# Kernel optimization log

Measured on AMD Instinct MI355X. Metric: run time of the kernel, lower is better.

Reference implementation:

```python
import jax, jax.numpy as jnp
import numpy as np

N, E, B = 50000, 400000, 8
ND, ED, H, L = 32, 16, 128, 3

def setup_inputs() -> dict:
    key = jax.random.key(0)
    ks = jax.random.split(key, 32)
    s = 0.05
    inp = {
        'x': jax.random.normal(ks[0], (N, ND), jnp.float32),
        'edge_attr': jax.random.normal(ks[1], (E, ED), jnp.float32),
        'global_feature': jax.random.normal(ks[2], (B, 1), jnp.float32),
        'edge_index': jax.random.randint(ks[3], (2, E), 0, N, jnp.int64),
        'batch': jnp.sort(jax.random.randint(ks[4], (N,), 0, B, jnp.int64)),
        # embeddings
        'Wn': jax.random.normal(ks[5], (ND, H), jnp.float32) * s,
        'bn': jnp.zeros((H,), jnp.float32),
        'We': jax.random.normal(ks[6], (ED, H), jnp.float32) * s,
        'be': jnp.zeros((H,), jnp.float32),
        'Wg': jax.random.normal(ks[7], (1, H), jnp.float32) * s,
        'bg': jnp.zeros((H,), jnp.float32),
        # message-passing layers (stacked over L)
        'mW1': jax.random.normal(ks[8], (L, 3 * H, H), jnp.float32) * s,
        'mb1': jnp.zeros((L, H), jnp.float32),
        'mW2': jax.random.normal(ks[9], (L, H, H), jnp.float32) * s,
        'mb2': jnp.zeros((L, H), jnp.float32),
        'uW1': jax.random.normal(ks[10], (L, 2 * H, H), jnp.float32) * s,
        'ub1': jnp.zeros((L, H), jnp.float32),
        'uW2': jax.random.normal(ks[11], (L, H, H), jnp.float32) * s,
        'ub2': jnp.zeros((L, H), jnp.float32),
        # readout MLP
        'rW1': jax.random.normal(ks[12], (2 * H, H), jnp.float32) * s,
        'rb1': jnp.zeros((H,), jnp.float32),
        'rW2': jax.random.normal(ks[13], (H, H // 2), jnp.float32) * s,
        'rb2': jnp.zeros((H // 2,), jnp.float32),
        'rW3': jax.random.normal(ks[14], (H // 2, 1), jnp.float32) * s,
        'rb3': jnp.zeros((1,), jnp.float32),
    }
    return inp

def reference(x, edge_attr, global_feature, Wn, bn, We, be, Wg, bg,
              mW1, mb1, mW2, mb2, uW1, ub1, uW2, ub2,
              rW1, rb1, rW2, rb2, rW3, rb3, edge_index, batch):
    h = x @ Wn + bn                      # [N,H]
    e = edge_attr @ We + be              # [E,H]
    g = global_feature @ Wg + bg         # [B,H]
    src, dst = edge_index[0], edge_index[1]  # PyG: x_j=source, x_i=target, aggregate at target
    for l in range(L):
        m_in = jnp.concatenate([h[dst], h[src], e], axis=1)            # [E,3H]
        m = jax.nn.relu(m_in @ mW1[l] + mb1[l]) @ mW2[l] + mb2[l]       # [E,H]
        aggr = jax.ops.segment_sum(m, dst, num_segments=N)              # [N,H]
        u_in = jnp.concatenate([h, aggr], axis=1)                       # [N,2H]
        upd = jax.nn.relu(u_in @ uW1[l] + ub1[l]) @ uW2[l] + ub2[l]
        h = h + upd
    counts = jax.ops.segment_sum(jnp.ones((N,), h.dtype), batch, num_segments=B)
    pooled = jax.ops.segment_sum(h, batch, num_segments=B) / jnp.maximum(counts, 1.0)[:, None]
    final = jnp.concatenate([pooled, g], axis=1)                        # [B,2H]
    out = jax.nn.relu(final @ rW1 + rb1)
    out = jax.nn.relu(out @ rW2 + rb2)
    return out @ rW3 + rb3                                              # [B,1]
```

## Files before the change

### kernel.cpp

```cpp
#include <hip/hip_runtime.h>

#define NN 50000
#define NPAD 50048
#define NBLK 391
#define NE 400000
#define NBATCH 8
#define NDIM 32
#define EDIM 16
#define H 128
#define NLAYERS 3
#define CHUNK_ELEMS 4096
#define NODE_CHUNKS 24
#define ZW_CHUNK 8192
#define NSB 196
#define ZEB 128

typedef __attribute__((ext_vector_type(8))) __bf16 bf16x8;
typedef __attribute__((ext_vector_type(16))) float f32x16;
typedef __attribute__((ext_vector_type(8))) short short8;
typedef __attribute__((ext_vector_type(2))) float v2f;

__device__ __forceinline__ void block_sync_lds() {
  asm volatile("s_waitcnt lgkmcnt(0)\ns_barrier" ::: "memory");
}
__device__ __forceinline__ void wait_lds() {
  asm volatile("s_waitcnt lgkmcnt(0)" ::: "memory");
}
__device__ __forceinline__ v2f bf2f(unsigned u) {
  v2f r;
  r.x = __uint_as_float(u << 16);
  r.y = __uint_as_float(u & 0xffff0000u);
  return r;
}

__global__ __launch_bounds__(128) void embed_nodes_kernel(
    const float* __restrict__ x, const float* __restrict__ Wn,
    const float* __restrict__ bn, __bf16* __restrict__ hb) {
  __shared__ float Ws[NDIM * H];
  __shared__ float xs[16 * NDIM];
  int j = threadIdx.x;
  int nbase = blockIdx.x * 16;
  for (int r = 0; r < NDIM; ++r) Ws[r * H + j] = Wn[r * H + j];
#pragma unroll
  for (int t = 0; t < 4; ++t) {
    int f = j + t * 128;
    xs[f] = x[nbase * NDIM + f];
  }
  __syncthreads();
  float b = bn[j];
  for (int nn = 0; nn < 16; ++nn) {
    float acc = b;
#pragma unroll
    for (int k = 0; k < NDIM; ++k)
      acc = fmaf(xs[nn * NDIM + k], Ws[k * H + j], acc);
    hb[(size_t)(nbase + nn) * H + j] = (__bf16)acc;
  }
}

__global__ __launch_bounds__(256) void degree_kernel(const int* __restrict__ ei,
                                                     int* __restrict__ deg) {
  int e = blockIdx.x * 256 + threadIdx.x;
  if (e < NE) atomicAdd(&deg[ei[NE + e]], 1);
}

__global__ __launch_bounds__(256) void scan1_kernel(const int* __restrict__ deg,
                                                    int* __restrict__ bsum) {
  __shared__ int ws[4];
  int i = blockIdx.x * 256 + threadIdx.x;
  int lane = threadIdx.x & 63, wid = threadIdx.x >> 6;
  int v = (i < NN) ? deg[i] : 0;
#pragma unroll
  for (int off = 32; off; off >>= 1) v += __shfl_down(v, off);
  if (lane == 0) ws[wid] = v;
  __syncthreads();
  if (threadIdx.x == 0) bsum[blockIdx.x] = ws[0] + ws[1] + ws[2] + ws[3];
}

__global__ __launch_bounds__(256) void scan2_kernel(const int* __restrict__ bsum,
                                                    int* __restrict__ boff) {
  __shared__ int s[256];
  int t = threadIdx.x;
  int v = (t < NSB) ? bsum[t] : 0;
  s[t] = v;
  __syncthreads();
  for (int off = 1; off < 256; off <<= 1) {
    int u = (t >= off) ? s[t - off] : 0;
    __syncthreads();
    s[t] += u;
    __syncthreads();
  }
  if (t < NSB) boff[t] = s[t] - v;
}

__global__ __launch_bounds__(256) void scan3_kernel(const int* __restrict__ deg,
                                                    const int* __restrict__ boff,
                                                    int* __restrict__ cursor) {
  __shared__ int wsum[4], woff[4];
  int i = blockIdx.x * 256 + threadIdx.x;
  int lane = threadIdx.x & 63, wid = threadIdx.x >> 6;
  int orig = (i < NN) ? deg[i] : 0;
  int v = orig;
#pragma unroll
  for (int off = 1; off < 64; off <<= 1) {
    int u = __shfl_up(v, off);
    if (lane >= off) v += u;
  }
  if (lane == 63) wsum[wid] = v;
  __syncthreads();
  if (threadIdx.x == 0) {
    int r = 0;
#pragma unroll
    for (int w = 0; w < 4; ++w) {
      woff[w] = r;
      r += wsum[w];
    }
  }
  __syncthreads();
  if (i < NN) cursor[i] = (v - orig) + woff[wid] + boff[blockIdx.x];
}

__global__ __launch_bounds__(256) void scatter_kernel(
    const int* __restrict__ ei, int* __restrict__ cursor,
    int* __restrict__ srcSrt, int* __restrict__ eidSrt) {
  int e = blockIdx.x * 256 + threadIdx.x;
  if (e < NE) {
    int d = ei[NE + e];
    int pos = atomicAdd(&cursor[d], 1);
    srcSrt[pos] = ei[e];
    eidSrt[pos] = e;
  }
}

__global__ __launch_bounds__(256) void gather_ea_kernel(
    const float* __restrict__ ea, const int* __restrict__ eidSrt,
    __bf16* __restrict__ eaSrt) {
  int fl = blockIdx.x * 256 + threadIdx.x;
  if (fl < NE) {
    int e = eidSrt[fl];
    const float4* ep = (const float4*)(ea + (size_t)e * EDIM);
    __bf16* op = eaSrt + (size_t)fl * EDIM;
#pragma unroll
    for (int q = 0; q < 4; ++q) {
      float4 v = ep[q];
      op[q * 4 + 0] = (__bf16)v.x;
      op[q * 4 + 1] = (__bf16)v.y;
      op[q * 4 + 2] = (__bf16)v.z;
      op[q * 4 + 3] = (__bf16)v.w;
    }
  }
}

__global__ __launch_bounds__(256) void precomp_zw_kernel(
    const float* __restrict__ mW1, __bf16* __restrict__ ZW) {
  int l = blockIdx.x / 8;
  int c = blockIdx.x % 8;
  int tid = threadIdx.x;
  const float* w1 = mW1 + (size_t)l * 384 * H;
  __bf16* dst = ZW + ((size_t)l * 8 + c) * ZW_CHUNK;
  for (int it = 0; it < 32; ++it) {
    int flat = it * 256 + tid;
    int j = flat & 7;
    int lane = (flat >> 3) & 63;
    int nt = (flat >> 9) & 7;
    int hilo = flat >> 12;
    int k = c * 16 + ((lane >> 5) << 3) + j;
    int n = nt * 32 + (lane & 31);
    float w = (n < 128) ? w1[(size_t)k * H + n]
                        : w1[(size_t)(128 + k) * H + (n - 128)];
    __bf16 hi = (__bf16)w;
    __bf16 lo = (__bf16)(w - (float)hi);
    dst[flat] = hilo ? lo : hi;
  }
}

__global__ __launch_bounds__(128) void precomp_wef_kernel(
    const float* __restrict__ mW1, const float* __restrict__ mb1,
    const float* __restrict__ We, const float* __restrict__ be,
    float* __restrict__ Wef, float* __restrict__ bm) {
  int l = blockIdx.x;
  int n = threadIdx.x;
  const float* w1 = mW1 + (size_t)l * 384 * H;
  float acc[EDIM];
#pragma unroll
  for (int i = 0; i < EDIM; ++i) acc[i] = 0.f;
  float accb = 0.f;
  for (int c = 0; c < H; ++c) {
    float wv = w1[(size_t)(256 + c) * H + n];
    accb = fmaf(be[c], wv, accb);
#pragma unroll
    for (int i = 0; i < EDIM; ++i)
      acc[i] = fmaf(We[i * H + c], wv, acc[i]);
  }
#pragma unroll
  for (int i = 0; i < EDIM; ++i)
    Wef[((size_t)l * EDIM + i) * H + n] = acc[i];
  bm[l * H + n] = mb1[l * H + n] + accb;
}

__global__ __launch_bounds__(256) void precomp_wefs_kernel(
    const float* __restrict__ Wef, __bf16* __restrict__ WefS) {
  int l = blockIdx.x;
  int tid = threadIdx.x;
  int nt = tid >> 6, lane = tid & 63;
  int n = nt * 32 + (lane & 31);
  int half = lane >> 5;
  const float* wl = Wef + (size_t)l * EDIM * H;
  __bf16* dst = WefS + (size_t)l * CHUNK_ELEMS;
#pragma unroll
  for (int j = 0; j < 8; ++j) {
    int k = half * 8 + j;
    float w = wl[(size_t)k * H + n];
    __bf16 hi = (__bf16)w;
    __bf16 lo = (__bf16)(w - (float)hi);
    dst[((0 * 4 + nt) * 64 + lane) * 8 + j] = hi;
    dst[((1 * 4 + nt) * 64 + lane) * 8 + j] = lo;
  }
}

__global__ __launch_bounds__(128) void precomp_wu_kernel(
    const float* __restrict__ uW1, const float* __restrict__ mW2,
    const float* __restrict__ mb2, float* __restrict__ Wu,
    float* __restrict__ va) {
  int l = blockIdx.x / 257;
  int r = blockIdx.x % 257;
  int j = threadIdx.x;
  const float* u1 = uW1 + (size_t)l * 256 * H;
  if (r < 128) {
    Wu[((size_t)l * 256 + r) * H + j] = u1[(size_t)r * H + j];
  } else if (r < 256) {
    int i = r - 128;
    const float* m2 = mW2 + ((size_t)l * H + i) * H;
    float s = 0.f;
    for (int c = 0; c < H; ++c)
      s = fmaf(m2[c], u1[(size_t)(128 + c) * H + j], s);
    Wu[((size_t)l * 256 + r) * H + j] = s;
  } else {
    float s = 0.f;
    for (int c = 0; c < H; ++c)
      s = fmaf(mb2[l * H + c], u1[(size_t)(128 + c) * H + j], s);
    va[l * H + j] = s;
  }
}

__global__ __launch_bounds__(256) void precomp_wns_kernel(
    const float* __restrict__ Wu, const float* __restrict__ uW2,
    __bf16* __restrict__ WnS) {
  int l = blockIdx.x / NODE_CHUNKS;
  int c = blockIdx.x % NODE_CHUNKS;
  int tid = threadIdx.x;
  int nt = tid >> 6, lane = tid & 63;
  int n = nt * 32 + (lane & 31);
  int half = lane >> 5;
  __bf16* dst = WnS + ((size_t)l * NODE_CHUNKS + c) * CHUNK_ELEMS;
#pragma unroll
  for (int j = 0; j < 8; ++j) {
    float w;
    if (c < 16) {
      int k = c * 16 + half * 8 + j;
      w = Wu[((size_t)l * 256 + k) * H + n];
    } else {
      int k = (c - 16) * 16 + half * 8 + j;
      w = uW2[((size_t)l * H + k) * H + n];
    }
    __bf16 hi = (__bf16)w;
    __bf16 lo = (__bf16)(w - (float)hi);
    dst[((0 * 4 + nt) * 64 + lane) * 8 + j] = hi;
    dst[((1 * 4 + nt) * 64 + lane) * 8 + j] = lo;
  }
}

__global__ __launch_bounds__(256) void zdzs_kernel(
    const __bf16* __restrict__ hb, const __bf16* __restrict__ ZW,
    const float* __restrict__ bm, __bf16* __restrict__ z) {
  __shared__ __align__(16) __bf16 Bt[2][ZW_CHUNK];
  int tid = threadIdx.x;
  int wid = tid >> 6, lane = tid & 63, m = lane & 31, half = lane >> 5;
  int nb = blockIdx.x * 128;
  int row = nb + wid * 32 + m;
  const __bf16* aH = hb + (size_t)row * H + half * 8;
  const short8* gW = (const short8*)ZW;
  short8* sB0 = (short8*)&Bt[0][0];
  short8* sB1 = (short8*)&Bt[1][0];
#pragma unroll
  for (int q = 0; q < 4; ++q) sB0[tid + q * 256] = gW[tid + q * 256];
  short8 p0 = gW[1024 + tid], p1 = gW[1024 + tid + 256];
  short8 p2 = gW[1024 + tid + 512], p3 = gW[1024 + tid + 768];
  f32x16 acc[8];
#pragma unroll
  for (int nt = 0; nt < 8; ++nt)
#pragma unroll
    for (int r = 0; r < 16; ++r) acc[nt][r] = 0.f;
  bf16x8 a = *(const bf16x8*)aH;
  block_sync_lds();

  for (int s = 0; s < 8; ++s) {
    int buf = s & 1;
    bf16x8 na = a;
    if (s + 1 < 8) na = *(const bf16x8*)(aH + (s + 1) * 16);
    if (s + 1 < 8) {
      short8* sb = buf ? sB0 : sB1;
      sb[tid] = p0;
      sb[tid + 256] = p1;
      sb[tid + 512] = p2;
      sb[tid + 768] = p3;
      if (s + 2 < 8) {
        p0 = gW[(size_t)(s + 2) * 1024 + tid];
        p1 = gW[(size_t)(s + 2) * 1024 + tid + 256];
        p2 = gW[(size_t)(s + 2) * 1024 + tid + 512];
        p3 = gW[(size_t)(s + 2) * 1024 + tid + 768];
      }
    }
    const __bf16* bb = &Bt[buf][0];
#pragma unroll
    for (int nt = 0; nt < 8; ++nt) {
      bf16x8 bh = *(const bf16x8*)&bb[((0 * 8 + nt) * 64 + lane) * 8];
      bf16x8 bl = *(const bf16x8*)&bb[((1 * 8 + nt) * 64 + lane) * 8];
      acc[nt] = __builtin_amdgcn_mfma_f32_32x32x16_bf16(a, bh, acc[nt], 0, 0, 0);
      acc[nt] = __builtin_amdgcn_mfma_f32_32x32x16_bf16(a, bl, acc[nt], 0, 0, 0);
    }
    a = na;
    if (s + 1 < 8) block_sync_lds();
  }

  float bmv[4];
#pragma unroll
  for (int nt = 0; nt < 4; ++nt) bmv[nt] = bm[nt * 32 + m];
#pragma unroll
  for (int nt = 0; nt < 8; ++nt) {
    float bias = (nt < 4) ? bmv[nt] : 0.f;
#pragma unroll
    for (int r = 0; r < 16; ++r) {
      int rowi = (r & 3) + 8 * (r >> 2) + 4 * half;
      z[(size_t)(nb + wid * 32 + rowi) * 256 + nt * 32 + m] =
          (__bf16)(acc[nt][r] + bias);
    }
  }
}

__global__ __launch_bounds__(256) void ze_kernel(
    const __bf16* __restrict__ eaSrt, const __bf16* __restrict__ WefS,
    __bf16* __restrict__ zePre) {
  __shared__ __align__(16) __bf16 Bf[CHUNK_ELEMS];
  int tid = threadIdx.x;
  ((short8*)Bf)[tid] = ((const short8*)WefS)[tid];
  ((short8*)Bf)[tid + 256] = ((const short8*)WefS)[tid + 256];
  int wid = tid >> 6, lane = tid & 63, m = lane & 31, half = lane >> 5;
  int ebase = blockIdx.x * ZEB + wid * 32;
  bf16x8 a = *(const bf16x8*)(eaSrt + (size_t)(ebase + m) * EDIM + half * 8);
  f32x16 acc[4];
#pragma unroll
  for (int nt = 0; nt < 4; ++nt)
#pragma unroll
    for (int r = 0; r < 16; ++r) acc[nt][r] = 0.f;
  block_sync_lds();
#pragma unroll
  for (int nt = 0; nt < 4; ++nt) {
    bf16x8 bh = *(const bf16x8*)&Bf[((0 * 4 + nt) * 64 + lane) * 8];
    bf16x8 bl = *(const bf16x8*)&Bf[((1 * 4 + nt) * 64 + lane) * 8];
    acc[nt] = __builtin_amdgcn_mfma_f32_32x32x16_bf16(a, bh, acc[nt], 0, 0, 0);
    acc[nt] = __builtin_amdgcn_mfma_f32_32x32x16_bf16(a, bl, acc[nt], 0, 0, 0);
  }
#pragma unroll
  for (int nt = 0; nt < 4; ++nt) {
#pragma unroll
    for (int r = 0; r < 16; ++r) {
      int rowi = (r & 3) + 8 * (r >> 2) + 4 * half;
      zePre[(size_t)(ebase + rowi) * H + nt * 32 + m] = (__bf16)acc[nt][r];
    }
  }
}

__global__ __launch_bounds__(256) void edge_aggr_kernel(
    const __bf16* __restrict__ z, const int* __restrict__ srcSrt,
    const int* __restrict__ cend, const __bf16* __restrict__ zePre,
    float* __restrict__ aggrH) {
  int node = blockIdx.x * 4 + (threadIdx.x >> 6);
  int lane = threadIdx.x & 63;
  int c0 = lane * 2;
  int end = cend[node];
  int start = node ? cend[node - 1] : 0;
  v2f acc = {0.f, 0.f};
  if (start < end) {
    v2f zd = bf2f(*(const unsigned*)(z + (size_t)node * 256 + c0));
    int sArr[4];
#pragma unroll
    for (int p = 0; p < 4; ++p)
      if (start + p < end) sArr[p] = srcSrt[start + p];
    for (int e0 = start; e0 < end; e0 += 4) {
      unsigned zsb[4], zeb[4];
#pragma unroll
      for (int p = 0; p < 4; ++p) {
        if (e0 + p < end) {
          zsb[p] = *(const unsigned*)(z + (size_t)sArr[p] * 256 + 128 + c0);
          zeb[p] = *(const unsigned*)(zePre + (size_t)(e0 + p) * H + c0);
        }
      }
#pragma unroll
      for (int p = 0; p < 4; ++p)
        if (e0 + 4 + p < end) sArr[p] = srcSrt[e0 + 4 + p];
#pragma unroll
      for (int p = 0; p < 4; ++p) {
        if (e0 + p < end) {
          v2f t = zd + bf2f(zsb[p]) + bf2f(zeb[p]);
          acc.x += fmaxf(t.x, 0.f);
          acc.y += fmaxf(t.y, 0.f);
        }
      }
    }
  }
  *(v2f*)(aggrH + (size_t)node * H + c0) = acc;
}

__global__ __launch_bounds__(256) void node_update_mfma_kernel(
    __bf16* __restrict__ hb, const float* __restrict__ aggrH,
    const int* __restrict__ deg, const __bf16* __restrict__ WnS,
    const float* __restrict__ ub1, const float* __restrict__ va,
    const float* __restrict__ ub2) {
  __shared__ __align__(16) __bf16 Bt[2][CHUNK_ELEMS];
  __shared__ __bf16 hid[2][32][132];
  __shared__ float degS[64];
  int tid = threadIdx.x;
  int nb = blockIdx.x * 64;
  if (tid < 64) degS[tid] = (float)deg[nb + tid];
  int wid = tid >> 6, lane = tid & 63, m = lane & 31, half = lane >> 5;
  int rg = wid & 1;
  int nh = wid >> 1;
  int row = nb + rg * 32 + m;
  const __bf16* aHb = hb + (size_t)row * H + half * 8;
  const float* aG = aggrH + (size_t)row * H + half * 8;
  const short8* gW = (const short8*)WnS;
  short8* sB0 = (short8*)&Bt[0][0];
  short8* sB1 = (short8*)&Bt[1][0];
  sB0[tid] = gW[tid];
  sB0[tid + 256] = gW[tid + 256];
  short8 p0 = gW[512 + tid], p1 = gW[512 + tid + 256];
  float bv1[2], bva[2];
#pragma unroll
  for (int ntl = 0; ntl < 2; ++ntl) {
    int nt = nh * 2 + ntl;
    bv1[ntl] = ub1[nt * 32 + m];
    bva[ntl] = va[nt * 32 + m];
  }
  f32x16 acc[2];
#pragma unroll
  for (int ntl = 0; ntl < 2; ++ntl)
#pragma unroll
    for (int r = 0; r < 16; ++r) acc[ntl][r] = 0.f;
  bf16x8 acur = *(const bf16x8*)aHb;
  block_sync_lds();

  for (int s = 0; s < 16; ++s) {
    int buf = s & 1;
    bf16x8 anext = acur;
    if (s + 1 < 16) {
      int sp = s + 1;
      if (sp < 8) {
        anext = *(const bf16x8*)(aHb + sp * 16);
      } else {
        const float* pp = aG + (sp - 8) * 16;
        float4 f0 = *(const float4*)pp;
        float4 f1 = *(const float4*)(pp + 4);
        float af[8] = {f0.x, f0.y, f0.z, f0.w, f1.x, f1.y, f1.z, f1.w};
#pragma unroll
        for (int j = 0; j < 8; ++j) anext[j] = (__bf16)af[j];
      }
    }
    {
      short8* sb = buf ? sB0 : sB1;
      sb[tid] = p0;
      sb[tid + 256] = p1;
      if (s + 2 < NODE_CHUNKS) {
        p0 = gW[(size_t)(s + 2) * 512 + tid];
        p1 = gW[(size_t)(s + 2) * 512 + tid + 256];
      }
    }
    const __bf16* bb = &Bt[buf][0];
#pragma unroll
    for (int ntl = 0; ntl < 2; ++ntl) {
      int nt = nh * 2 + ntl;
      bf16x8 bh = *(const bf16x8*)&bb[((0 * 4 + nt) * 64 + lane) * 8];
      bf16x8 bl = *(const bf16x8*)&bb[((1 * 4 + nt) * 64 + lane) * 8];
      acc[ntl] = __builtin_amdgcn_mfma_f32_32x32x16_bf16(acur, bh, acc[ntl], 0, 0, 0);
      acc[ntl] = __builtin_amdgcn_mfma_f32_32x32x16_bf16(acur, bl, acc[ntl], 0, 0, 0);
    }
    acur = anext;
    block_sync_lds();
  }

#pragma unroll
  for (int ntl = 0; ntl < 2; ++ntl) {
    int nt = nh * 2 + ntl;
#pragma unroll
    for (int r = 0; r < 16; ++r) {
      int rowi = (r & 3) + 8 * (r >> 2) + 4 * half;
      float v = acc[ntl][r] + bv1[ntl] + degS[rg * 32 + rowi] * bva[ntl];
      hid[rg][rowi][nt * 32 + m] = (__bf16)fmaxf(v, 0.f);
      acc[ntl][r] = 0.f;
    }
  }
  block_sync_lds();

  for (int s = 16; s < NODE_CHUNKS; ++s) {
    int buf = s & 1;
    if (s + 1 < NODE_CHUNKS) {
      short8* sb = buf ? sB0 : sB1;
      sb[tid] = p0;
      sb[tid + 256] = p1;
      if (s + 2 < NODE_CHUNKS) {
        p0 = gW[(size_t)(s + 2) * 512 + tid];
        p1 = gW[(size_t)(s + 2) * 512 + tid + 256];
      }
    }
    bf16x8 ah = *(const bf16x8*)&hid[rg][m][(s - 16) * 16 + half * 8];
    const __bf16* bb = &Bt[buf][0];
#pragma unroll
    for (int ntl = 0; ntl < 2; ++ntl) {
      int nt = nh * 2 + ntl;
      bf16x8 bh = *(const bf16x8*)&bb[((0 * 4 + nt) * 64 + lane) * 8];
      bf16x8 bl = *(const bf16x8*)&bb[((1 * 4 + nt) * 64 + lane) * 8];
      acc[ntl] = __builtin_amdgcn_mfma_f32_32x32x16_bf16(ah, bh, acc[ntl], 0, 0, 0);
      acc[ntl] = __builtin_amdgcn_mfma_f32_32x32x16_bf16(ah, bl, acc[ntl], 0, 0, 0);
    }
    if (s + 1 < NODE_CHUNKS) block_sync_lds();
  }

#pragma unroll
  for (int ntl = 0; ntl < 2; ++ntl) {
    int nt = nh * 2 + ntl;
    float b2 = ub2[nt * 32 + m];
#pragma unroll
    for (int r = 0; r < 16; ++r) {
      int rowi = (r & 3) + 8 * (r >> 2) + 4 * half;
      size_t idx = (size_t)(nb + rg * 32 + rowi) * H + nt * 32 + m;
      float hv = (float)hb[idx];
      hb[idx] = (__bf16)(hv + acc[ntl][r] + b2);
    }
  }
}

__global__ __launch_bounds__(256) void pool_kernel(
    const __bf16* __restrict__ hb, const int* __restrict__ batch,
    float* __restrict__ pooled, int* __restrict__ counts) {
  __shared__ float pS[NBATCH * H];
  __shared__ int cS[NBATCH];
  int tid = threadIdx.x;
  for (int i = tid; i < NBATCH * H; i += 256) pS[i] = 0.f;
  if (tid < NBATCH) cS[tid] = 0;
  __syncthreads();
  int c = tid & 15;
  int r0 = tid >> 4;
  int nbase = blockIdx.x * 128;
  v2f acc4[4] = {{0.f, 0.f}, {0.f, 0.f}, {0.f, 0.f}, {0.f, 0.f}};
  int cnt = 0;
  int cur = -1;
#pragma unroll
  for (int i = 0; i < 8; ++i) {
    int n = nbase + i * 16 + r0;
    if (n >= NN) break;
    int b = batch[n];
    if (b != cur) {
      if (cur >= 0) {
#pragma unroll
        for (int q = 0; q < 4; ++q) {
          atomicAdd(&pS[cur * H + c * 8 + q * 2], acc4[q].x);
          atomicAdd(&pS[cur * H + c * 8 + q * 2 + 1], acc4[q].y);
          acc4[q].x = 0.f;
          acc4[q].y = 0.f;
        }
        if (c == 0) atomicAdd(&cS[cur], cnt);
        cnt = 0;
      }
      cur = b;
    }
    uint4 v = *(const uint4*)(hb + (size_t)n * H + c * 8);
    acc4[0] += bf2f(v.x);
    acc4[1] += bf2f(v.y);
    acc4[2] += bf2f(v.z);
    acc4[3] += bf2f(v.w);
    cnt++;
  }
  if (cur >= 0) {
#pragma unroll
    for (int q = 0; q < 4; ++q) {
      atomicAdd(&pS[cur * H + c * 8 + q * 2], acc4[q].x);
      atomicAdd(&pS[cur * H + c * 8 + q * 2 + 1], acc4[q].y);
    }
    if (c == 0) atomicAdd(&cS[cur], cnt);
  }
  __syncthreads();
  for (int i = tid; i < NBATCH * H; i += 256) {
    float v = pS[i];
    if (v != 0.f) unsafeAtomicAdd(&pooled[i], v);
  }
  if (tid < NBATCH) {
    int cv = cS[tid];
    if (cv) atomicAdd(&counts[tid], cv);
  }
}

__global__ __launch_bounds__(128) void readout_kernel(
    const float* __restrict__ pooled, const int* __restrict__ counts,
    const float* __restrict__ gf, const float* __restrict__ Wg,
    const float* __restrict__ bg, const float* __restrict__ rW1,
    const float* __restrict__ rb1, const float* __restrict__ rW2,
    const float* __restrict__ rb2, const float* __restrict__ rW3,
    const float* __restrict__ rb3, float* __restrict__ out) {
  __shared__ float fin[256];
  __shared__ float t1[128];
  __shared__ float t2[64];
  int j = threadIdx.x;
  int b = blockIdx.x;
  float cnt = (float)counts[b];
  if (cnt < 1.f) cnt = 1.f;
  fin[j] = pooled[b * H + j] / cnt;
  fin[H + j] = fmaf(gf[b], Wg[j], bg[j]);
  __syncthreads();
  float a = rb1[j];
  for (int k = 0; k < 256; ++k) a = fmaf(fin[k], rW1[k * H + j], a);
  t1[j] = fmaxf(a, 0.f);
  __syncthreads();
  if (j < 64) {
    float a2 = rb2[j];
    for (int k = 0; k < 128; ++k) a2 = fmaf(t1[k], rW2[k * 64 + j], a2);
    t2[j] = fmaxf(a2, 0.f);
  }
  __syncthreads();
  if (j < 64) {
    float p = t2[j] * rW3[j];
#pragma unroll
    for (int off = 32; off; off >>= 1) p += __shfl_down(p, off);
    if (j == 0) out[b] = p + rb3[0];
  }
}

extern "C" void kernel_launch(void* const* d_in, const int* in_sizes, int n_in,
                              void* d_out, int out_size, void* d_ws, size_t ws_size,
                              hipStream_t stream) {
  const float* x   = (const float*)d_in[0];
  const float* ea  = (const float*)d_in[1];
  const float* gf  = (const float*)d_in[2];
  const int*   ei  = (const int*)d_in[3];
  const int*   bat = (const int*)d_in[4];
  const float* Wn  = (const float*)d_in[5];
  const float* bn  = (const float*)d_in[6];
  const float* We  = (const float*)d_in[7];
  const float* be  = (const float*)d_in[8];
  const float* Wg  = (const float*)d_in[9];
  const float* bg  = (const float*)d_in[10];
  const float* mW1 = (const float*)d_in[11];
  const float* mb1 = (const float*)d_in[12];
  const float* mW2 = (const float*)d_in[13];
  const float* mb2 = (const float*)d_in[14];
  const float* uW1 = (const float*)d_in[15];
  const float* ub1 = (const float*)d_in[16];
  const float* uW2 = (const float*)d_in[17];
  const float* ub2 = (const float*)d_in[18];
  const float* rW1 = (const float*)d_in[19];
  const float* rb1 = (const float*)d_in[20];
  const float* rW2 = (const float*)d_in[21];
  const float* rb2 = (const float*)d_in[22];
  const float* rW3 = (const float*)d_in[23];
  const float* rb3 = (const float*)d_in[24];

  char* p = (char*)d_ws;
  __bf16* hb     = (__bf16*)p; p += (size_t)NPAD * H * 2;
  float*  aggrH  = (float*)p;  p += (size_t)NPAD * H * 4;
  __bf16* z      = (__bf16*)p; p += (size_t)NPAD * 256 * 2;
  __bf16* zePre  = (__bf16*)p; p += (size_t)NE * H * 2;
  __bf16* eaSrt  = (__bf16*)p; p += (size_t)NE * EDIM * 2;
  int*    srcSrt = (int*)p;    p += (size_t)NE * 4;
  int*    eidSrt = (int*)p;    p += (size_t)NE * 4;
  __bf16* ZW     = (__bf16*)p; p += (size_t)NLAYERS * 8 * ZW_CHUNK * 2;
  __bf16* WnS    = (__bf16*)p; p += (size_t)NLAYERS * NODE_CHUNKS * CHUNK_ELEMS * 2;
  __bf16* WefS   = (__bf16*)p; p += (size_t)NLAYERS * CHUNK_ELEMS * 2;
  float*  Wef    = (float*)p;  p += (size_t)NLAYERS * EDIM * H * 4;
  float*  bm     = (float*)p;  p += (size_t)NLAYERS * H * 4;
  float*  Wu     = (float*)p;  p += (size_t)NLAYERS * 256 * H * 4;
  float*  va     = (float*)p;  p += (size_t)NLAYERS * H * 4;
  int*    deg    = (int*)p;    p += (size_t)NPAD * 4;
  int*    cursor = (int*)p;    p += (size_t)NPAD * 4;
  int*    bsum   = (int*)p;    p += 256 * 4;
  int*    boff   = (int*)p;    p += 256 * 4;
  float*  pooled = (float*)p;  p += (size_t)NBATCH * H * 4;
  int*    counts = (int*)p;    p += 64;

  hipMemsetAsync(deg, 0, (size_t)NPAD * 4, stream);
  hipMemsetAsync(cursor, 0, (size_t)NPAD * 4, stream);
  hipMemsetAsync(pooled, 0, (size_t)NBATCH * H * 4, stream);
  hipMemsetAsync(counts, 0, 64, stream);

  embed_nodes_kernel<<<NN / 16, 128, 0, stream>>>(x, Wn, bn, hb);
  degree_kernel<<<(NE + 255) / 256, 256, 0, stream>>>(ei, deg);
  scan1_kernel<<<NSB, 256, 0, stream>>>(deg, bsum);
  scan2_kernel<<<1, 256, 0, stream>>>(bsum, boff);
  scan3_kernel<<<NSB, 256, 0, stream>>>(deg, boff, cursor);
  scatter_kernel<<<(NE + 255) / 256, 256, 0, stream>>>(ei, cursor, srcSrt, eidSrt);
  gather_ea_kernel<<<(NE + 255) / 256, 256, 0, stream>>>(ea, eidSrt, eaSrt);
  precomp_zw_kernel<<<NLAYERS * 8, 256, 0, stream>>>(mW1, ZW);
  precomp_wef_kernel<<<NLAYERS, 128, 0, stream>>>(mW1, mb1, We, be, Wef, bm);
  precomp_wefs_kernel<<<NLAYERS, 256, 0, stream>>>(Wef, WefS);
  precomp_wu_kernel<<<NLAYERS * 257, 128, 0, stream>>>(uW1, mW2, mb2, Wu, va);
  precomp_wns_kernel<<<NLAYERS * NODE_CHUNKS, 256, 0, stream>>>(Wu, uW2, WnS);

  for (int l = 0; l < NLAYERS; ++l) {
    zdzs_kernel<<<NBLK, 256, 0, stream>>>(
        hb, ZW + (size_t)l * 8 * ZW_CHUNK, bm + (size_t)l * H, z);
    ze_kernel<<<NE / ZEB, 256, 0, stream>>>(
        eaSrt, WefS + (size_t)l * CHUNK_ELEMS, zePre);
    edge_aggr_kernel<<<NPAD / 4, 256, 0, stream>>>(
        z, srcSrt, cursor, zePre, aggrH);
    node_update_mfma_kernel<<<NPAD / 64, 256, 0, stream>>>(
        hb, aggrH, deg, WnS + (size_t)l * NODE_CHUNKS * CHUNK_ELEMS,
        ub1 + (size_t)l * H, va + (size_t)l * H, ub2 + (size_t)l * H);
  }

  pool_kernel<<<NPAD / 128, 256, 0, stream>>>(hb, bat, pooled, counts);
  readout_kernel<<<NBATCH, 128, 0, stream>>>(pooled, counts, gf, Wg, bg, rW1,
                                             rb1, rW2, rb2, rW3, rb3,
                                             (float*)d_out);
}
```

Before: 563.8 us.

## Fuse edge-attribute projection into edge aggregation and store aggregates in bf16

Removes the per-layer ze_kernel, which wrote a bf16 E×H edge projection, and instead computes the 16-wide edge-attribute dot products inline in edge_aggr_kernel from fp32 sorted edge attributes and LDS-staged Wef. This avoids writing and re-reading a 400000×128 intermediate every layer, at the cost of extra FMAs per edge and channel. Source index and edge id are packed into one int2 array, the gather loop is rewritten as a software-pipelined single-edge loop, and the aggregate buffer becomes bf16 so the node-update kernel loads bf16 directly. Storing aggregates in bf16 may reduce precision.

```diff
diff --git a/kernel.cpp b/kernel.cpp
--- a/kernel.cpp
+++ b/kernel.cpp
@@ -13,7 +13,6 @@
 #define NODE_CHUNKS 24
 #define ZW_CHUNK 8192
 #define NSB 196
-#define ZEB 128
 
 typedef __attribute__((ext_vector_type(8))) __bf16 bf16x8;
 typedef __attribute__((ext_vector_type(16))) float f32x16;
@@ -22,9 +21,6 @@
 
 __device__ __forceinline__ void block_sync_lds() {
   asm volatile("s_waitcnt lgkmcnt(0)\ns_barrier" ::: "memory");
-}
-__device__ __forceinline__ void wait_lds() {
-  asm volatile("s_waitcnt lgkmcnt(0)" ::: "memory");
 }
 __device__ __forceinline__ v2f bf2f(unsigned u) {
   v2f r;
@@ -121,32 +117,25 @@
 
 __global__ __launch_bounds__(256) void scatter_kernel(
     const int* __restrict__ ei, int* __restrict__ cursor,
-    int* __restrict__ srcSrt, int* __restrict__ eidSrt) {
+    int2* __restrict__ seSrt) {
   int e = blockIdx.x * 256 + threadIdx.x;
   if (e < NE) {
     int d = ei[NE + e];
     int pos = atomicAdd(&cursor[d], 1);
-    srcSrt[pos] = ei[e];
-    eidSrt[pos] = e;
-  }
-}
-
-__global__ __launch_bounds__(256) void gather_ea_kernel(
-    const float* __restrict__ ea, const int* __restrict__ eidSrt,
-    __bf16* __restrict__ eaSrt) {
+    seSrt[pos] = make_int2(ei[e], e);
+  }
+}
+
+__global__ __launch_bounds__(256) void gather_eaF_kernel(
+    const float* __restrict__ ea, const int2* __restrict__ seSrt,
+    float* __restrict__ eaF) {
   int fl = blockIdx.x * 256 + threadIdx.x;
   if (fl < NE) {
-    int e = eidSrt[fl];
+    int e = seSrt[fl].y;
     const float4* ep = (const float4*)(ea + (size_t)e * EDIM);
-    __bf16* op = eaSrt + (size_t)fl * EDIM;
-#pragma unroll
-    for (int q = 0; q < 4; ++q) {
-      float4 v = ep[q];
-      op[q * 4 + 0] = (__bf16)v.x;
-      op[q * 4 + 1] = (__bf16)v.y;
-      op[q * 4 + 2] = (__bf16)v.z;
-      op[q * 4 + 3] = (__bf16)v.w;
-    }
+    float4* op = (float4*)(eaF + (size_t)fl * EDIM);
+#pragma unroll
+    for (int q = 0; q < 4; ++q) op[q] = ep[q];
   }
 }
 
@@ -195,26 +184,6 @@
   for (int i = 0; i < EDIM; ++i)
     Wef[((size_t)l * EDIM + i) * H + n] = acc[i];
   bm[l * H + n] = mb1[l * H + n] + accb;
-}
-
-__global__ __launch_bounds__(256) void precomp_wefs_kernel(
-    const float* __restrict__ Wef, __bf16* __restrict__ WefS) {
-  int l = blockIdx.x;
-  int tid = threadIdx.x;
-  int nt = tid >> 6, lane = tid & 63;
-  int n = nt * 32 + (lane & 31);
-  int half = lane >> 5;
-  const float* wl = Wef + (size_t)l * EDIM * H;
-  __bf16* dst = WefS + (size_t)l * CHUNK_ELEMS;
-#pragma unroll
-  for (int j = 0; j < 8; ++j) {
-    int k = half * 8 + j;
-    float w = wl[(size_t)k * H + n];
-    __bf16 hi = (__bf16)w;
-    __bf16 lo = (__bf16)(w - (float)hi);
-    dst[((0 * 4 + nt) * 64 + lane) * 8 + j] = hi;
-    dst[((1 * 4 + nt) * 64 + lane) * 8 + j] = lo;
-  }
 }
 
 __global__ __launch_bounds__(128) void precomp_wu_kernel(
@@ -337,82 +306,72 @@
   }
 }
 
-__global__ __launch_bounds__(256) void ze_kernel(
-    const __bf16* __restrict__ eaSrt, const __bf16* __restrict__ WefS,
-    __bf16* __restrict__ zePre) {
-  __shared__ __align__(16) __bf16 Bf[CHUNK_ELEMS];
+__global__ __launch_bounds__(256) void edge_aggr_kernel(
+    const __bf16* __restrict__ z, const int2* __restrict__ seSrt,
+    const int* __restrict__ cend, const float* __restrict__ eaF,
+    const float* __restrict__ WefL, __bf16* __restrict__ aggrB) {
+  __shared__ float wefS[EDIM * H];
   int tid = threadIdx.x;
-  ((short8*)Bf)[tid] = ((const short8*)WefS)[tid];
-  ((short8*)Bf)[tid + 256] = ((const short8*)WefS)[tid + 256];
-  int wid = tid >> 6, lane = tid & 63, m = lane & 31, half = lane >> 5;
-  int ebase = blockIdx.x * ZEB + wid * 32;
-  bf16x8 a = *(const bf16x8*)(eaSrt + (size_t)(ebase + m) * EDIM + half * 8);
-  f32x16 acc[4];
-#pragma unroll
-  for (int nt = 0; nt < 4; ++nt)
-#pragma unroll
-    for (int r = 0; r < 16; ++r) acc[nt][r] = 0.f;
-  block_sync_lds();
-#pragma unroll
-  for (int nt = 0; nt < 4; ++nt) {
-    bf16x8 bh = *(const bf16x8*)&Bf[((0 * 4 + nt) * 64 + lane) * 8];
-    bf16x8 bl = *(const bf16x8*)&Bf[((1 * 4 + nt) * 64 + lane) * 8];
-    acc[nt] = __builtin_amdgcn_mfma_f32_32x32x16_bf16(a, bh, acc[nt], 0, 0, 0);
-    acc[nt] = __builtin_amdgcn_mfma_f32_32x32x16_bf16(a, bl, acc[nt], 0, 0, 0);
-  }
-#pragma unroll
-  for (int nt = 0; nt < 4; ++nt) {
-#pragma unroll
-    for (int r = 0; r < 16; ++r) {
-      int rowi = (r & 3) + 8 * (r >> 2) + 4 * half;
-      zePre[(size_t)(ebase + rowi) * H + nt * 32 + m] = (__bf16)acc[nt][r];
-    }
-  }
-}
-
-__global__ __launch_bounds__(256) void edge_aggr_kernel(
-    const __bf16* __restrict__ z, const int* __restrict__ srcSrt,
-    const int* __restrict__ cend, const __bf16* __restrict__ zePre,
-    float* __restrict__ aggrH) {
-  int node = blockIdx.x * 4 + (threadIdx.x >> 6);
-  int lane = threadIdx.x & 63;
+#pragma unroll
+  for (int q = 0; q < 8; ++q) wefS[tid + q * 256] = WefL[tid + q * 256];
+  __syncthreads();
+  int node = blockIdx.x * 4 + (tid >> 6);
+  int lane = tid & 63;
   int c0 = lane * 2;
+  v2f wef[16];
+#pragma unroll
+  for (int k = 0; k < 16; ++k) wef[k] = *(const v2f*)(&wefS[k * H + c0]);
   int end = cend[node];
   int start = node ? cend[node - 1] : 0;
   v2f acc = {0.f, 0.f};
   if (start < end) {
     v2f zd = bf2f(*(const unsigned*)(z + (size_t)node * 256 + c0));
-    int sArr[4];
-#pragma unroll
-    for (int p = 0; p < 4; ++p)
-      if (start + p < end) sArr[p] = srcSrt[start + p];
-    for (int e0 = start; e0 < end; e0 += 4) {
-      unsigned zsb[4], zeb[4];
-#pragma unroll
-      for (int p = 0; p < 4; ++p) {
-        if (e0 + p < end) {
-          zsb[p] = *(const unsigned*)(z + (size_t)sArr[p] * 256 + 128 + c0);
-          zeb[p] = *(const unsigned*)(zePre + (size_t)(e0 + p) * H + c0);
-        }
+    int sB = (start + 1 < end) ? seSrt[start + 1].x : 0;
+    unsigned zcur =
+        *(const unsigned*)(z + (size_t)seSrt[start].x * 256 + 128 + c0);
+    const float4* ep = (const float4*)(eaF + (size_t)start * EDIM);
+    float4 a0 = ep[0], a1 = ep[1], a2 = ep[2], a3 = ep[3];
+    for (int e = start; e < end; ++e) {
+      int sC = (e + 2 < end) ? seSrt[e + 2].x : 0;
+      unsigned znx = 0;
+      float4 n0 = a0, n1 = a1, n2 = a2, n3 = a3;
+      if (e + 1 < end) {
+        znx = *(const unsigned*)(z + (size_t)sB * 256 + 128 + c0);
+        const float4* np = (const float4*)(eaF + (size_t)(e + 1) * EDIM);
+        n0 = np[0]; n1 = np[1]; n2 = np[2]; n3 = np[3];
       }
-#pragma unroll
-      for (int p = 0; p < 4; ++p)
-        if (e0 + 4 + p < end) sArr[p] = srcSrt[e0 + 4 + p];
-#pragma unroll
-      for (int p = 0; p < 4; ++p) {
-        if (e0 + p < end) {
-          v2f t = zd + bf2f(zsb[p]) + bf2f(zeb[p]);
-          acc.x += fmaxf(t.x, 0.f);
-          acc.y += fmaxf(t.y, 0.f);
-        }
-      }
-    }
-  }
-  *(v2f*)(aggrH + (size_t)node * H + c0) = acc;
+      v2f t = zd + bf2f(zcur);
+      t.x = fmaf(a0.x, wef[0].x, t.x);   t.y = fmaf(a0.x, wef[0].y, t.y);
+      t.x = fmaf(a0.y, wef[1].x, t.x);   t.y = fmaf(a0.y, wef[1].y, t.y);
+      t.x = fmaf(a0.z, wef[2].x, t.x);   t.y = fmaf(a0.z, wef[2].y, t.y);
+      t.x = fmaf(a0.w, wef[3].x, t.x);   t.y = fmaf(a0.w, wef[3].y, t.y);
+      t.x = fmaf(a1.x, wef[4].x, t.x);   t.y = fmaf(a1.x, wef[4].y, t.y);
+      t.x = fmaf(a1.y, wef[5].x, t.x);   t.y = fmaf(a1.y, wef[5].y, t.y);
+      t.x = fmaf(a1.z, wef[6].x, t.x);   t.y = fmaf(a1.z, wef[6].y, t.y);
+      t.x = fmaf(a1.w, wef[7].x, t.x);   t.y = fmaf(a1.w, wef[7].y, t.y);
+      t.x = fmaf(a2.x, wef[8].x, t.x);   t.y = fmaf(a2.x, wef[8].y, t.y);
+      t.x = fmaf(a2.y, wef[9].x, t.x);   t.y = fmaf(a2.y, wef[9].y, t.y);
+      t.x = fmaf(a2.z, wef[10].x, t.x);  t.y = fmaf(a2.z, wef[10].y, t.y);
+      t.x = fmaf(a2.w, wef[11].x, t.x);  t.y = fmaf(a2.w, wef[11].y, t.y);
+      t.x = fmaf(a3.x, wef[12].x, t.x);  t.y = fmaf(a3.x, wef[12].y, t.y);
+      t.x = fmaf(a3.y, wef[13].x, t.x);  t.y = fmaf(a3.y, wef[13].y, t.y);
+      t.x = fmaf(a3.z, wef[14].x, t.x);  t.y = fmaf(a3.z, wef[14].y, t.y);
+      t.x = fmaf(a3.w, wef[15].x, t.x);  t.y = fmaf(a3.w, wef[15].y, t.y);
+      acc.x += fmaxf(t.x, 0.f);
+      acc.y += fmaxf(t.y, 0.f);
+      zcur = znx;
+      sB = sC;
+      a0 = n0; a1 = n1; a2 = n2; a3 = n3;
+    }
+  }
+  union { __bf16 b[2]; unsigned u; } pk;
+  pk.b[0] = (__bf16)acc.x;
+  pk.b[1] = (__bf16)acc.y;
+  *(unsigned*)(aggrB + (size_t)node * H + c0) = pk.u;
 }
 
 __global__ __launch_bounds__(256) void node_update_mfma_kernel(
-    __bf16* __restrict__ hb, const float* __restrict__ aggrH,
+    __bf16* __restrict__ hb, const __bf16* __restrict__ aggrB,
     const int* __restrict__ deg, const __bf16* __restrict__ WnS,
     const float* __restrict__ ub1, const float* __restrict__ va,
     const float* __restrict__ ub2) {
@@ -427,7 +386,7 @@
   int nh = wid >> 1;
   int row = nb + rg * 32 + m;
   const __bf16* aHb = hb + (size_t)row * H + half * 8;
-  const float* aG = aggrH + (size_t)row * H + half * 8;
+  const __bf16* aGb = aggrB + (size_t)row * H + half * 8;
   const short8* gW = (const short8*)WnS;
   short8* sB0 = (short8*)&Bt[0][0];
   short8* sB1 = (short8*)&Bt[1][0];
@@ -454,16 +413,8 @@
     bf16x8 anext = acur;
     if (s + 1 < 16) {
       int sp = s + 1;
-      if (sp < 8) {
-        anext = *(const bf16x8*)(aHb + sp * 16);
-      } else {
-        const float* pp = aG + (sp - 8) * 16;
-        float4 f0 = *(const float4*)pp;
-        float4 f1 = *(const float4*)(pp + 4);
-        float af[8] = {f0.x, f0.y, f0.z, f0.w, f1.x, f1.y, f1.z, f1.w};
-#pragma unroll
-        for (int j = 0; j < 8; ++j) anext[j] = (__bf16)af[j];
-      }
+      anext = (sp < 8) ? *(const bf16x8*)(aHb + sp * 16)
+                       : *(const bf16x8*)(aGb + (sp - 8) * 16);
     }
     {
       short8* sb = buf ? sB0 : sB1;
@@ -664,15 +615,12 @@
 
   char* p = (char*)d_ws;
   __bf16* hb     = (__bf16*)p; p += (size_t)NPAD * H * 2;
-  float*  aggrH  = (float*)p;  p += (size_t)NPAD * H * 4;
+  __bf16* aggrB  = (__bf16*)p; p += (size_t)NPAD * H * 2;
   __bf16* z      = (__bf16*)p; p += (size_t)NPAD * 256 * 2;
-  __bf16* zePre  = (__bf16*)p; p += (size_t)NE * H * 2;
-  __bf16* eaSrt  = (__bf16*)p; p += (size_t)NE * EDIM * 2;
-  int*    srcSrt = (int*)p;    p += (size_t)NE * 4;
-  int*    eidSrt = (int*)p;    p += (size_t)NE * 4;
+  float*  eaF    = (float*)p;  p += (size_t)NE * EDIM * 4;
+  int2*   seSrt  = (int2*)p;   p += (size_t)NE * 8;
   __bf16* ZW     = (__bf16*)p; p += (size_t)NLAYERS * 8 * ZW_CHUNK * 2;
   __bf16* WnS    = (__bf16*)p; p += (size_t)NLAYERS * NODE_CHUNKS * CHUNK_ELEMS * 2;
-  __bf16* WefS   = (__bf16*)p; p += (size_t)NLAYERS * CHUNK_ELEMS * 2;
   float*  Wef    = (float*)p;  p += (size_t)NLAYERS * EDIM * H * 4;
   float*  bm     = (float*)p;  p += (size_t)NLAYERS * H * 4;
   float*  Wu     = (float*)p;  p += (size_t)NLAYERS * 256 * H * 4;
@@ -694,23 +642,20 @@
   scan1_kernel<<<NSB, 256, 0, stream>>>(deg, bsum);
   scan2_kernel<<<1, 256, 0, stream>>>(bsum, boff);
   scan3_kernel<<<NSB, 256, 0, stream>>>(deg, boff, cursor);
-  scatter_kernel<<<(NE + 255) / 256, 256, 0, stream>>>(ei, cursor, srcSrt, eidSrt);
-  gather_ea_kernel<<<(NE + 255) / 256, 256, 0, stream>>>(ea, eidSrt, eaSrt);
+  scatter_kernel<<<(NE + 255) / 256, 256, 0, stream>>>(ei, cursor, seSrt);
+  gather_eaF_kernel<<<(NE + 255) / 256, 256, 0, stream>>>(ea, seSrt, eaF);
   precomp_zw_kernel<<<NLAYERS * 8, 256, 0, stream>>>(mW1, ZW);
   precomp_wef_kernel<<<NLAYERS, 128, 0, stream>>>(mW1, mb1, We, be, Wef, bm);
-  precomp_wefs_kernel<<<NLAYERS, 256, 0, stream>>>(Wef, WefS);
   precomp_wu_kernel<<<NLAYERS * 257, 128, 0, stream>>>(uW1, mW2, mb2, Wu, va);
   precomp_wns_kernel<<<NLAYERS * NODE_CHUNKS, 256, 0, stream>>>(Wu, uW2, WnS);
 
   for (int l = 0; l < NLAYERS; ++l) {
     zdzs_kernel<<<NBLK, 256, 0, stream>>>(
         hb, ZW + (size_t)l * 8 * ZW_CHUNK, bm + (size_t)l * H, z);
-    ze_kernel<<<NE / ZEB, 256, 0, stream>>>(
-        eaSrt, WefS + (size_t)l * CHUNK_ELEMS, zePre);
     edge_aggr_kernel<<<NPAD / 4, 256, 0, stream>>>(
-        z, srcSrt, cursor, zePre, aggrH);
+        z, seSrt, cursor, eaF, Wef + (size_t)l * EDIM * H, aggrB);
     node_update_mfma_kernel<<<NPAD / 64, 256, 0, stream>>>(
-        hb, aggrH, deg, WnS + (size_t)l * NODE_CHUNKS * CHUNK_ELEMS,
+        hb, aggrB, deg, WnS + (size_t)l * NODE_CHUNKS * CHUNK_ELEMS,
         ub1 + (size_t)l * H, va + (size_t)l * H, ub2 + (size_t)l * H);
   }
 
```

After: 598.5 us. +6.1%, slower.
